# Performance work log

Measured on AMD Instinct MI355X. Metric: run time of the kernel, lower is better.

Reference implementation:

```python
import jax, jax.numpy as jnp
import numpy as np

NUM_EXPERTS = 8
K = 2
N_EMBD = 1024
HIDDEN = 4 * N_EMBD
BATCH = 2
SEQ = 1024
LB_SCALE = 0.01
NOISY_STD = 1.0
INIT_S = 0.02


def setup_inputs() -> dict:
    key = jax.random.key(0)
    ks = jax.random.split(key, 8)
    D, H, E = N_EMBD, HIDDEN, NUM_EXPERTS
    return {
        "x": jax.random.normal(ks[0], (BATCH, SEQ, D), jnp.float32),
        "noise": jax.random.normal(ks[1], (BATCH, SEQ, E), jnp.float32),  # torch.randn_like(logits)
        "gate_w": jax.random.normal(ks[2], (E, D), jnp.float32) * INIT_S,
        "noise_weight": jnp.zeros((E,), jnp.float32),  # initialized to zeros in the module
        "w1": jax.random.normal(ks[3], (E, H, D), jnp.float32) * INIT_S,
        "b1": jnp.zeros((E, H), jnp.float32),
        "w2": jax.random.normal(ks[4], (E, H, D), jnp.float32) * INIT_S,
        "b2": jnp.zeros((E, H), jnp.float32),
        "wp": jax.random.normal(ks[5], (E, D, H), jnp.float32) * INIT_S,
        "bp": jnp.zeros((E, D), jnp.float32),
    }


def reference(x, noise, gate_w, noise_weight, w1, b1, w2, b2, wp, bp):
    B, S, D = x.shape
    E = gate_w.shape[0]

    # ---- TopKGateParallel ----
    logits = jnp.einsum('bsd,ed->bse', x, gate_w)           # [B,S,E]
    gate_weights = jax.nn.softmax(logits, axis=-1)
    gw_mean = gate_weights.reshape(-1, E).mean(axis=0)       # [E]
    load_balance_loss = jnp.mean((gw_mean - 1.0 / E) ** 2) * LB_SCALE  # mse vs uniform

    logits_noisy = logits + (noise * NOISY_STD) * noise_weight
    top_v, top_i = jax.lax.top_k(logits_noisy, K)            # [B,S,K]
    # scatter top-k logits into a -inf sea, then softmax -> zeros at non-topk slots
    topk_mask = jnp.sum(jax.nn.one_hot(top_i, E, dtype=jnp.float32), axis=-2) > 0  # [B,S,E]
    sparse_logits = jnp.where(topk_mask, logits_noisy, -jnp.inf)
    top_k_gated_weights = jax.nn.softmax(sparse_logits, axis=-1)  # [B,S,E]

    # ---- expert compute + weighted combine (world_size=1: all experts local) ----
    x_flat = x.reshape(B * S, D)                              # [T,D]
    w_flat = top_k_gated_weights.reshape(B * S, E)            # [T,E]
    y = jnp.zeros_like(x_flat)
    for e in range(E):  # fixed small set of experts
        h = x_flat @ w1[e].T + b1[e]                          # [T,H]
        g = x_flat @ w2[e].T + b2[e]                          # [T,H]
        out_e = (h * jax.nn.silu(g)) @ wp[e].T + bp[e]        # [T,D]
        y = y + w_flat[:, e:e + 1] * out_e
    y = y.reshape(B, S, D)
    return y, load_balance_loss
```

## Files before the change

kernel.cpp:

```cpp
#include <hip/hip_runtime.h>

#define TOK 2048
#define DIM 1024
#define HID 4096
#define NE 8
#define KSPLIT 4
#define T2MAX 12

typedef unsigned short u16;
typedef __attribute__((ext_vector_type(8))) short s16x8;
typedef __attribute__((ext_vector_type(4))) short s16x4;
typedef __attribute__((ext_vector_type(4))) float f32x4;

__device__ __forceinline__ u16 f2b(float f) {
  unsigned u = __builtin_bit_cast(unsigned, f);
  unsigned r = (u + 0x7fffu + ((u >> 16) & 1u)) >> 16;
  return (u16)r;
}

__device__ __forceinline__ void gld_lds16(const void* g, void* l) {
  __builtin_amdgcn_global_load_lds((const __attribute__((address_space(1))) void*)g,
                                   (__attribute__((address_space(3))) void*)l, 16, 0, 0);
}

__global__ __launch_bounds__(256) void k_gate(const float* __restrict__ x,
    const float* __restrict__ noise, const float* __restrict__ gw,
    const float* __restrict__ nw,
    int* __restrict__ tok_e, float* __restrict__ tok_w,
    int* __restrict__ bhist, float* __restrict__ bgw, u16* __restrict__ x16) {
  const int wid = threadIdx.x >> 6, lane = threadIdx.x & 63;
  const int t = blockIdx.x * 4 + wid;
  const float* xr = x + (size_t)t * DIM + lane * 16;
  float acc[NE];
#pragma unroll
  for (int e = 0; e < NE; ++e) acc[e] = 0.f;
  u16 xb[16];
#pragma unroll
  for (int j = 0; j < 4; ++j) {
    float4 xv = *(const float4*)(xr + j * 4);
    xb[j * 4 + 0] = f2b(xv.x); xb[j * 4 + 1] = f2b(xv.y);
    xb[j * 4 + 2] = f2b(xv.z); xb[j * 4 + 3] = f2b(xv.w);
#pragma unroll
    for (int e = 0; e < NE; ++e) {
      float4 gv = *(const float4*)(gw + e * DIM + lane * 16 + j * 4);
      acc[e] += xv.x * gv.x + xv.y * gv.y + xv.z * gv.z + xv.w * gv.w;
    }
  }
  *(s16x8*)(x16 + (size_t)t * DIM + lane * 16) = *(const s16x8*)xb;
  *(s16x8*)(x16 + (size_t)t * DIM + lane * 16 + 8) = *(const s16x8*)(xb + 8);
#pragma unroll
  for (int e = 0; e < NE; ++e) {
#pragma unroll
    for (int off = 32; off >= 1; off >>= 1) acc[e] += __shfl_xor(acc[e], off);
  }
  float m = acc[0];
#pragma unroll
  for (int e = 1; e < NE; ++e) m = fmaxf(m, acc[e]);
  float p[NE]; float s = 0.f;
#pragma unroll
  for (int e = 0; e < NE; ++e) { p[e] = expf(acc[e] - m); s += p[e]; }
  float inv = 1.f / s;
  float v[NE];
#pragma unroll
  for (int e = 0; e < NE; ++e) v[e] = acc[e] + noise[t * NE + e] * nw[e];
  float v0 = -3.4e38f, v1 = -3.4e38f; int i0 = 0, i1 = 0;
#pragma unroll
  for (int e = 0; e < NE; ++e) {
    float ve = v[e];
    if (ve > v0) { v1 = v0; i1 = i0; v0 = ve; i0 = e; }
    else if (ve > v1) { v1 = ve; i1 = e; }
  }
  float e1 = expf(v1 - v0);
  float den = 1.f + e1;
  float w0 = 1.f / den, w1v = e1 / den;

  __shared__ float pl[4][NE];
  __shared__ int el[4][2];
  if (lane == 0) {
#pragma unroll
    for (int e = 0; e < NE; ++e) pl[wid][e] = p[e] * inv;
    el[wid][0] = i0; el[wid][1] = i1;
    tok_e[t * 2] = i0; tok_e[t * 2 + 1] = i1;
    tok_w[t * 2] = w0; tok_w[t * 2 + 1] = w1v;
  }
  __syncthreads();
  if (threadIdx.x < NE) {
    const int e = threadIdx.x;
    float ps = pl[0][e] + pl[1][e] + pl[2][e] + pl[3][e];
    int h = 0;
#pragma unroll
    for (int j = 0; j < 4; ++j) {
      h += (el[j][0] == e);
      h += (el[j][1] == e);
    }
    bgw[blockIdx.x * NE + e] = ps;
    bhist[blockIdx.x * NE + e] = h;
  }
}

__global__ __launch_bounds__(512) void k_scan(const int* __restrict__ bhist,
    const float* __restrict__ bgw, int* __restrict__ blk_off, int* __restrict__ prefix,
    int* __restrict__ counts, int* __restrict__ tile_tab, float* __restrict__ loss_out) {
  const int i = threadIdx.x, lane = i & 63, wv = i >> 6;
  __shared__ int wsum[8];
  __shared__ float wfs[8];
  __shared__ int etot[8];
  __shared__ float fsum[8];
  for (int e = 0; e < NE; ++e) {
    int v = bhist[i * NE + e];
    int sc = v;
#pragma unroll
    for (int off = 1; off < 64; off <<= 1) {
      int u = __shfl_up(sc, off);
      if (lane >= off) sc += u;
    }
    float f = bgw[i * NE + e];
#pragma unroll
    for (int off = 32; off >= 1; off >>= 1) f += __shfl_xor(f, off);
    if (lane == 63) wsum[wv] = sc;
    if (lane == 0) wfs[wv] = f;
    __syncthreads();
    int base = 0;
    for (int w2 = 0; w2 < wv; ++w2) base += wsum[w2];
    blk_off[i * NE + e] = base + sc - v;
    if (i == 0) {
      float tf = 0.f;
      for (int w2 = 0; w2 < 8; ++w2) tf += wfs[w2];
      fsum[e] = tf;
    }
    if (i == 511) etot[e] = base + sc;
    __syncthreads();
  }
  if (i == 0) {
    int sacc = 0;
    float l = 0.f;
    int tt = 0;
#pragma unroll
    for (int e = 0; e < NE; ++e) { prefix[e] = sacc; counts[e] = etot[e]; sacc += etot[e]; }
    for (int e = 0; e < NE; ++e) {
      const int nmt = (etot[e] + 511) >> 9;
      for (int m2 = 0; m2 < nmt; ++m2) tile_tab[tt++] = (e << 16) | m2;
    }
    for (; tt < T2MAX; ++tt) tile_tab[tt] = -1;
#pragma unroll
    for (int e = 0; e < NE; ++e) {
      float d = fsum[e] * (1.f / TOK) - 0.125f;
      l += d * d;
    }
    *loss_out = l * (0.01f / NE);
  }
}

__global__ __launch_bounds__(256) void k_build(const int* __restrict__ tok_e,
    const float* __restrict__ tok_w, const int* __restrict__ prefix,
    const int* __restrict__ blk_off, int* __restrict__ ent, float* __restrict__ entw,
    int* __restrict__ inv) {
  const int t = blockIdx.x * 256 + threadIdx.x;
  const int g = t >> 2;
  const int base = (t & 3) * 2;
  int ee[8];
#pragma unroll
  for (int j = 0; j < 8; ++j) ee[j] = tok_e[g * 8 + j];
#pragma unroll
  for (int s = 0; s < 2; ++s) {
    const int e = ee[base + s];
    int rank = 0;
#pragma unroll
    for (int j = 0; j < 8; ++j) rank += (j < base + s) && (ee[j] == e);
    const int idx = prefix[e] + blk_off[g * NE + e] + rank;
    ent[idx] = t * 2 + s;
    entw[idx] = tok_w[t * 2 + s];
    inv[t * 2 + s] = idx;
  }
}

__global__ __launch_bounds__(512) void k_gemm1f(const u16* __restrict__ x16,
    const float* __restrict__ w1, const float* __restrict__ w2,
    const float* __restrict__ b1, const float* __restrict__ b2,
    const int* __restrict__ ent, const int* __restrict__ counts,
    const int* __restrict__ prefix, const int* __restrict__ tile_tab,
    u16* __restrict__ act) {
  const int tt = tile_tab[blockIdx.y];
  if (tt < 0) return;
  const int e = tt >> 16, mt = tt & 0xffff, nt = blockIdx.x;
  const int cnt = counts[e];
  const int pfx = prefix[e];
  const int tid = threadIdx.x, w = tid >> 6, l = tid & 63;

  __shared__ u16 smem[2][20480];

  const int cA = (tid & 3) ^ ((tid >> 3) & 3);
  const u16* srcA[4]; int dstA[4];
#pragma unroll
  for (int q = 0; q < 4; ++q) {
    const int rr = q * 128 + (tid >> 2);
    int g = mt * 512 + rr; if (g >= cnt) g = cnt - 1;
    srcA[q] = x16 + (size_t)(ent[pfx + g] >> 1) * DIM + cA * 8;
    dstA[q] = q * 4096 + tid * 8;
  }
  const int rB = tid >> 3, cB = tid & 7;
  const float* pB1 = w1 + ((size_t)e * HID + nt * 64 + rB) * DIM + cB * 4;
  const float* pB2 = w2 + ((size_t)e * HID + nt * 64 + rB) * DIM + cB * 4;
  const int pos8 = cB ^ (((rB >> 1) & 3) << 1);
  const int wb1 = 16384 + rB * 32 + pos8 * 4;
  const int wb2 = 18432 + rB * 32 + pos8 * 4;

  const int xs = ((l >> 4) ^ ((l >> 1) & 3)) * 8;
  const int ra = (w * 64 + (l & 15)) * 32;
  const int rbb = (l & 15) * 32;

  f32x4 acc1[4][4], acc2[4][4];
#pragma unroll
  for (int m = 0; m < 4; ++m)
#pragma unroll
    for (int n = 0; n < 4; ++n) {
      acc1[m][n] = (f32x4){0.f, 0.f, 0.f, 0.f};
      acc2[m][n] = (f32x4){0.f, 0.f, 0.f, 0.f};
    }

  f32x4 a0_, a1_;
  f32x4 b0_, b1_;

  auto LOADB = [&](f32x4& r0_, f32x4& r1_, int kt) {
    r0_ = *(const f32x4*)(pB1 + kt * 32);
    r1_ = *(const f32x4*)(pB2 + kt * 32);
  };
  auto STAGEA = [&](int buf, int kt) {
#pragma unroll
    for (int q = 0; q < 4; ++q) gld_lds16(srcA[q] + kt * 32, &smem[buf][dstA[q]]);
  };
  auto WRITEB = [&](int buf, const f32x4& r0_, const f32x4& r1_) {
    u16 u[8];
    u[0] = f2b(r0_[0]); u[1] = f2b(r0_[1]); u[2] = f2b(r0_[2]); u[3] = f2b(r0_[3]);
    u[4] = f2b(r1_[0]); u[5] = f2b(r1_[1]); u[6] = f2b(r1_[2]); u[7] = f2b(r1_[3]);
    *(s16x4*)&smem[buf][wb1] = *(const s16x4*)u;
    *(s16x4*)&smem[buf][wb2] = *(const s16x4*)(u + 4);
  };
  auto MSTEP = [&](int buf) {
    const u16* S = &smem[buf][0];
    s16x8 af[4];
#pragma unroll
    for (int m = 0; m < 4; ++m) af[m] = *(const s16x8*)(S + ra + m * 512 + xs);
    __builtin_amdgcn_s_setprio(1);
#pragma unroll
    for (int n = 0; n < 4; ++n) {
      s16x8 bf1 = *(const s16x8*)(S + 16384 + n * 512 + rbb + xs);
      s16x8 bf2 = *(const s16x8*)(S + 18432 + n * 512 + rbb + xs);
#pragma unroll
      for (int m = 0; m < 4; ++m) {
        acc1[m][n] = __builtin_amdgcn_mfma_f32_16x16x32_bf16(af[m], bf1, acc1[m][n], 0, 0, 0);
        acc2[m][n] = __builtin_amdgcn_mfma_f32_16x16x32_bf16(af[m], bf2, acc2[m][n], 0, 0, 0);
      }
    }
    __builtin_amdgcn_s_setprio(0);
  };

  const int NT = DIM / 32;
  LOADB(a0_, a1_, 0);
  STAGEA(0, 0);
  LOADB(b0_, b1_, 1);
  asm volatile("s_waitcnt vmcnt(2)" ::: "memory");
  __builtin_amdgcn_sched_barrier(0);
  WRITEB(0, a0_, a1_);
  STAGEA(1, 1);
  asm volatile("s_waitcnt lgkmcnt(0)" ::: "memory");
  __builtin_amdgcn_sched_barrier(0);
  __builtin_amdgcn_s_barrier();

  for (int kt = 0; kt < NT; kt += 2) {
    if (kt + 2 < NT) LOADB(a0_, a1_, kt + 2);
    MSTEP(0);
    __builtin_amdgcn_s_barrier();
    if (kt + 2 < NT) asm volatile("s_waitcnt vmcnt(2)" ::: "memory");
    else             asm volatile("s_waitcnt vmcnt(0)" ::: "memory");
    __builtin_amdgcn_sched_barrier(0);
    WRITEB(1, b0_, b1_);
    if (kt + 2 < NT) STAGEA(0, kt + 2);
    asm volatile("s_waitcnt lgkmcnt(0)" ::: "memory");
    __builtin_amdgcn_sched_barrier(0);
    __builtin_amdgcn_s_barrier();
    if (kt + 3 < NT) LOADB(b0_, b1_, kt + 3);
    MSTEP(1);
    if (kt + 2 < NT) {
      __builtin_amdgcn_s_barrier();
      if (kt + 3 < NT) asm volatile("s_waitcnt vmcnt(2)" ::: "memory");
      else             asm volatile("s_waitcnt vmcnt(0)" ::: "memory");
      __builtin_amdgcn_sched_barrier(0);
      WRITEB(0, a0_, a1_);
      if (kt + 3 < NT) STAGEA(1, kt + 3);
      asm volatile("s_waitcnt lgkmcnt(0)" ::: "memory");
      __builtin_amdgcn_sched_barrier(0);
      __builtin_amdgcn_s_barrier();
    }
  }

#pragma unroll
  for (int n = 0; n < 4; ++n) {
    const int col = nt * 64 + n * 16 + (l & 15);
    const float bb1 = b1[(size_t)e * HID + col];
    const float bb2 = b2[(size_t)e * HID + col];
#pragma unroll
    for (int m = 0; m < 4; ++m) {
#pragma unroll
      for (int r = 0; r < 4; ++r) {
        const int row = mt * 512 + w * 64 + m * 16 + (l >> 4) * 4 + r;
        if (row < cnt) {
          float h = acc1[m][n][r] + bb1;
          float g = acc2[m][n][r] + bb2;
          float a = h * g / (1.f + expf(-g));
          act[(size_t)(pfx + row) * HID + col] = f2b(a);
        }
      }
    }
  }
}

__global__ __launch_bounds__(512) void k_gemm2f(const u16* __restrict__ act,
    const float* __restrict__ wp, const float* __restrict__ bp,
    const float* __restrict__ entw, const int* __restrict__ counts,
    const int* __restrict__ prefix, const int* __restrict__ tile_tab,
    float* __restrict__ yp) {
  const int tt = tile_tab[blockIdx.y];
  if (tt < 0) return;
  const int e = tt >> 16, mt = tt & 0xffff;
  const int sk = blockIdx.z, nt = blockIdx.x;
  const int cnt = counts[e];
  const int pfx = prefix[e];
  const int tid = threadIdx.x, w = tid >> 6, l = tid & 63;

  __shared__ u16 smem[2][20480];

  const int kbase = sk * (HID / KSPLIT);
  const int cA = (tid & 3) ^ ((tid >> 3) & 3);
  const u16* srcA[4]; int dstA[4];
#pragma unroll
  for (int q = 0; q < 4; ++q) {
    const int rr = q * 128 + (tid >> 2);
    int g = mt * 512 + rr; if (g >= cnt) g = cnt - 1;
    srcA[q] = act + (size_t)(pfx + g) * HID + kbase + cA * 8;
    dstA[q] = q * 4096 + tid * 8;
  }
  const int rB = tid >> 2;
  const float* pB = wp + ((size_t)e * DIM + nt * 128 + rB) * HID + kbase + (tid & 3) * 8;
  const int c0 = ((tid & 3) * 2) ^ (((rB >> 1) & 3) << 1);
  const int c1 = ((tid & 3) * 2 + 1) ^ (((rB >> 1) & 3) << 1);
  const int wbB = 16384 + rB * 32;

  const int xs = ((l >> 4) ^ ((l >> 1) & 3)) * 8;
  const int ra = (w * 64 + (l & 15)) * 32;
  const int rbb = (l & 15) * 32;

  f32x4 acc[4][8];
#pragma unroll
  for (int m = 0; m < 4; ++m)
#pragma unroll
    for (int n = 0; n < 8; ++n) acc[m][n] = (f32x4){0.f, 0.f, 0.f, 0.f};

  f32x4 a0_, a1_;
  f32x4 b0_, b1_;

  auto LOADB = [&](f32x4& r0_, f32x4& r1_, int kt) {
    r0_ = *(const f32x4*)(pB + kt * 32);
    r1_ = *(const f32x4*)(pB + kt * 32 + 4);
  };
  auto STAGEA = [&](int buf, int kt) {
#pragma unroll
    for (int q = 0; q < 4; ++q) gld_lds16(srcA[q] + kt * 32, &smem[buf][dstA[q]]);
  };
  auto WRITEB = [&](int buf, const f32x4& r0_, const f32x4& r1_) {
    u16 u[8];
    u[0] = f2b(r0_[0]); u[1] = f2b(r0_[1]); u[2] = f2b(r0_[2]); u[3] = f2b(r0_[3]);
    u[4] = f2b(r1_[0]); u[5] = f2b(r1_[1]); u[6] = f2b(r1_[2]); u[7] = f2b(r1_[3]);
    *(s16x4*)&smem[buf][wbB + c0 * 4] = *(const s16x4*)u;
    *(s16x4*)&smem[buf][wbB + c1 * 4] = *(const s16x4*)(u + 4);
  };
  auto MSTEP = [&](int buf) {
    const u16* S = &smem[buf][0];
    s16x8 af[4];
#pragma unroll
    for (int m = 0; m < 4; ++m) af[m] = *(const s16x8*)(S + ra + m * 512 + xs);
    __builtin_amdgcn_s_setprio(1);
#pragma unroll
    for (int n = 0; n < 8; ++n) {
      s16x8 bf = *(const s16x8*)(S + 16384 + n * 512 + rbb + xs);
#pragma unroll
      for (int m = 0; m < 4; ++m)
        acc[m][n] = __builtin_amdgcn_mfma_f32_16x16x32_bf16(af[m], bf, acc[m][n], 0, 0, 0);
    }
    __builtin_amdgcn_s_setprio(0);
  };

  const int NT = HID / KSPLIT / 32;
  LOADB(a0_, a1_, 0);
  STAGEA(0, 0);
  LOADB(b0_, b1_, 1);
  asm volatile("s_waitcnt vmcnt(2)" ::: "memory");
  __builtin_amdgcn_sched_barrier(0);
  WRITEB(0, a0_, a1_);
  STAGEA(1, 1);
  asm volatile("s_waitcnt lgkmcnt(0)" ::: "memory");
  __builtin_amdgcn_sched_barrier(0);
  __builtin_amdgcn_s_barrier();

  for (int kt = 0; kt < NT; kt += 2) {
    if (kt + 2 < NT) LOADB(a0_, a1_, kt + 2);
    MSTEP(0);
    __builtin_amdgcn_s_barrier();
    if (kt + 2 < NT) asm volatile("s_waitcnt vmcnt(2)" ::: "memory");
    else             asm volatile("s_waitcnt vmcnt(0)" ::: "memory");
    __builtin_amdgcn_sched_barrier(0);
    WRITEB(1, b0_, b1_);
    if (kt + 2 < NT) STAGEA(0, kt + 2);
    asm volatile("s_waitcnt lgkmcnt(0)" ::: "memory");
    __builtin_amdgcn_sched_barrier(0);
    __builtin_amdgcn_s_barrier();
    if (kt + 3 < NT) LOADB(b0_, b1_, kt + 3);
    MSTEP(1);
    if (kt + 2 < NT) {
      __builtin_amdgcn_s_barrier();
      if (kt + 3 < NT) asm volatile("s_waitcnt vmcnt(2)" ::: "memory");
      else             asm volatile("s_waitcnt vmcnt(0)" ::: "memory");
      __builtin_amdgcn_sched_barrier(0);
      WRITEB(0, a0_, a1_);
      if (kt + 3 < NT) STAGEA(1, kt + 3);
      asm volatile("s_waitcnt lgkmcnt(0)" ::: "memory");
      __builtin_amdgcn_sched_barrier(0);
      __builtin_amdgcn_s_barrier();
    }
  }

#pragma unroll
  for (int n = 0; n < 8; ++n) {
    const int col = nt * 128 + n * 16 + (l & 15);
    const float bpv = (sk == 0) ? bp[(size_t)e * DIM + col] : 0.f;
#pragma unroll
    for (int m = 0; m < 4; ++m) {
#pragma unroll
      for (int r = 0; r < 4; ++r) {
        const int row = mt * 512 + w * 64 + m * 16 + (l >> 4) * 4 + r;
        if (row < cnt) {
          const int idx = pfx + row;
          yp[((size_t)sk * (TOK * 2) + idx) * DIM + col] = entw[idx] * (acc[m][n][r] + bpv);
        }
      }
    }
  }
}

__global__ __launch_bounds__(256) void k_final(const float* __restrict__ yp,
    const int* __restrict__ inv, float* __restrict__ out) {
  const int t = blockIdx.x;
  const int d = threadIdx.x * 4;
  const int i0 = inv[t * 2], i1 = inv[t * 2 + 1];
  float4 s = {0.f, 0.f, 0.f, 0.f};
#pragma unroll
  for (int sk = 0; sk < KSPLIT; ++sk) {
    float4 a = *(const float4*)(yp + ((size_t)sk * (TOK * 2) + i0) * DIM + d);
    float4 b = *(const float4*)(yp + ((size_t)sk * (TOK * 2) + i1) * DIM + d);
    s.x += a.x + b.x; s.y += a.y + b.y; s.z += a.z + b.z; s.w += a.w + b.w;
  }
  *(float4*)(out + (size_t)t * DIM + d) = s;
}

extern "C" void kernel_launch(void* const* d_in, const int* in_sizes, int n_in,
                              void* d_out, int out_size, void* d_ws, size_t ws_size,
                              hipStream_t stream) {
  const float* x      = (const float*)d_in[0];
  const float* noise  = (const float*)d_in[1];
  const float* gate_w = (const float*)d_in[2];
  const float* nw     = (const float*)d_in[3];
  const float* w1     = (const float*)d_in[4];
  const float* b1     = (const float*)d_in[5];
  const float* w2     = (const float*)d_in[6];
  const float* b2     = (const float*)d_in[7];
  const float* wp     = (const float*)d_in[8];
  const float* bp     = (const float*)d_in[9];
  float* out = (float*)d_out;
  char* ws = (char*)d_ws;

  const size_t SZ_X16 = (size_t)TOK * DIM * 2;
  const size_t SZ_ACT = (size_t)TOK * 2 * HID * 2;
  const size_t SZ_YP  = (size_t)KSPLIT * TOK * 2 * DIM * 4;

  u16* x16  = (u16*)ws;
  u16* act  = (u16*)(ws + SZ_X16);
  float* yp = (float*)(ws + SZ_X16 + SZ_ACT);
  char* meta = ws + SZ_X16 + SZ_ACT + SZ_YP;
  int*   tok_e    = (int*)(meta);
  float* tok_w    = (float*)(meta + 16384);
  int*   ent      = (int*)(meta + 32768);
  float* entw     = (float*)(meta + 49152);
  int*   bhist    = (int*)(meta + 65536);
  float* bgw      = (float*)(meta + 81920);
  int*   blk_off  = (int*)(meta + 98304);
  int*   inv      = (int*)(meta + 114688);
  int*   counts   = (int*)(meta + 131072);
  int*   prefix   = (int*)(meta + 131072 + 64);
  int*   tile_tab = (int*)(meta + 131072 + 128);

  k_gate<<<TOK / 4, 256, 0, stream>>>(x, noise, gate_w, nw, tok_e, tok_w, bhist, bgw, x16);
  k_scan<<<1, 512, 0, stream>>>(bhist, bgw, blk_off, prefix, counts, tile_tab,
                                out + (size_t)TOK * DIM);
  k_build<<<TOK / 256, 256, 0, stream>>>(tok_e, tok_w, prefix, blk_off, ent, entw, inv);
  k_gemm1f<<<dim3(HID / 64, T2MAX), 512, 0, stream>>>(x16, w1, w2, b1, b2, ent,
                                                      counts, prefix, tile_tab, act);
  k_gemm2f<<<dim3(DIM / 128, T2MAX, KSPLIT), 512, 0, stream>>>(act, wp, bp, entw,
                                                               counts, prefix, tile_tab, yp);
  k_final<<<TOK, 256, 0, stream>>>(yp, inv, out);
}
```

Baseline: 322.3 us.

## Triple-buffer LDS in both expert GEMMs with one barrier per k-step

```diff
diff --git a/kernel.cpp b/kernel.cpp
--- a/kernel.cpp
+++ b/kernel.cpp
@@ -5,7 +5,7 @@
 #define HID 4096
 #define NE 8
 #define KSPLIT 4
-#define T2MAX 12
+#define T2MAX 16
 
 typedef unsigned short u16;
 typedef __attribute__((ext_vector_type(8))) short s16x8;
@@ -139,7 +139,7 @@
     for (int e = 0; e < NE; ++e) { prefix[e] = sacc; counts[e] = etot[e]; sacc += etot[e]; }
     for (int e = 0; e < NE; ++e) {
       const int nmt = (etot[e] + 511) >> 9;
-      for (int m2 = 0; m2 < nmt; ++m2) tile_tab[tt++] = (e << 16) | m2;
+      for (int m2 = 0; m2 < nmt && tt < T2MAX; ++m2) tile_tab[tt++] = (e << 16) | m2;
     }
     for (; tt < T2MAX; ++tt) tile_tab[tt] = -1;
 #pragma unroll
@@ -187,23 +187,21 @@
   const int pfx = prefix[e];
   const int tid = threadIdx.x, w = tid >> 6, l = tid & 63;
 
-  __shared__ u16 smem[2][20480];
+  __shared__ u16 smem[61440];
 
   const int cA = (tid & 3) ^ ((tid >> 3) & 3);
-  const u16* srcA[4]; int dstA[4];
+  const u16* srcA[4];
 #pragma unroll
   for (int q = 0; q < 4; ++q) {
     const int rr = q * 128 + (tid >> 2);
     int g = mt * 512 + rr; if (g >= cnt) g = cnt - 1;
     srcA[q] = x16 + (size_t)(ent[pfx + g] >> 1) * DIM + cA * 8;
-    dstA[q] = q * 4096 + tid * 8;
   }
   const int rB = tid >> 3, cB = tid & 7;
   const float* pB1 = w1 + ((size_t)e * HID + nt * 64 + rB) * DIM + cB * 4;
   const float* pB2 = w2 + ((size_t)e * HID + nt * 64 + rB) * DIM + cB * 4;
   const int pos8 = cB ^ (((rB >> 1) & 3) << 1);
-  const int wb1 = 16384 + rB * 32 + pos8 * 4;
-  const int wb2 = 18432 + rB * 32 + pos8 * 4;
+  const int wbOff = rB * 32 + pos8 * 4;
 
   const int xs = ((l >> 4) ^ ((l >> 1) & 3)) * 8;
   const int ra = (w * 64 + (l & 15)) * 32;
@@ -218,81 +216,78 @@
       acc2[m][n] = (f32x4){0.f, 0.f, 0.f, 0.f};
     }
 
-  f32x4 a0_, a1_;
-  f32x4 b0_, b1_;
-
-  auto LOADB = [&](f32x4& r0_, f32x4& r1_, int kt) {
-    r0_ = *(const f32x4*)(pB1 + kt * 32);
-    r1_ = *(const f32x4*)(pB2 + kt * 32);
-  };
-  auto STAGEA = [&](int buf, int kt) {
-#pragma unroll
-    for (int q = 0; q < 4; ++q) gld_lds16(srcA[q] + kt * 32, &smem[buf][dstA[q]]);
-  };
-  auto WRITEB = [&](int buf, const f32x4& r0_, const f32x4& r1_) {
-    u16 u[8];
-    u[0] = f2b(r0_[0]); u[1] = f2b(r0_[1]); u[2] = f2b(r0_[2]); u[3] = f2b(r0_[3]);
-    u[4] = f2b(r1_[0]); u[5] = f2b(r1_[1]); u[6] = f2b(r1_[2]); u[7] = f2b(r1_[3]);
-    *(s16x4*)&smem[buf][wb1] = *(const s16x4*)u;
-    *(s16x4*)&smem[buf][wb2] = *(const s16x4*)(u + 4);
-  };
-  auto MSTEP = [&](int buf) {
-    const u16* S = &smem[buf][0];
-    s16x8 af[4];
-#pragma unroll
-    for (int m = 0; m < 4; ++m) af[m] = *(const s16x8*)(S + ra + m * 512 + xs);
-    __builtin_amdgcn_s_setprio(1);
-#pragma unroll
-    for (int n = 0; n < 4; ++n) {
-      s16x8 bf1 = *(const s16x8*)(S + 16384 + n * 512 + rbb + xs);
-      s16x8 bf2 = *(const s16x8*)(S + 18432 + n * 512 + rbb + xs);
-#pragma unroll
-      for (int m = 0; m < 4; ++m) {
-        acc1[m][n] = __builtin_amdgcn_mfma_f32_16x16x32_bf16(af[m], bf1, acc1[m][n], 0, 0, 0);
-        acc2[m][n] = __builtin_amdgcn_mfma_f32_16x16x32_bf16(af[m], bf2, acc2[m][n], 0, 0, 0);
-      }
-    }
-    __builtin_amdgcn_s_setprio(0);
-  };
+  f32x4 rA0, rA1;
+  f32x4 rB0, rB1;
+
+#define LB1(R0, R1, KT) { R0 = *(const f32x4*)(pB1 + (KT) * 32); R1 = *(const f32x4*)(pB2 + (KT) * 32); }
+#define ST1(NXT, KT) { _Pragma("unroll") for (int q = 0; q < 4; ++q) \
+    gld_lds16(srcA[q] + (KT) * 32, &smem[(NXT) * 16384 + q * 4096 + tid * 8]); }
+#define WB1(WBUF, R0, R1) { u16 u_[8]; \
+    u_[0] = f2b(R0[0]); u_[1] = f2b(R0[1]); u_[2] = f2b(R0[2]); u_[3] = f2b(R0[3]); \
+    u_[4] = f2b(R1[0]); u_[5] = f2b(R1[1]); u_[6] = f2b(R1[2]); u_[7] = f2b(R1[3]); \
+    *(s16x4*)&smem[49152 + (WBUF) * 4096 + wbOff] = *(const s16x4*)u_; \
+    *(s16x4*)&smem[49152 + (WBUF) * 4096 + 2048 + wbOff] = *(const s16x4*)(u_ + 4); }
+#define MS1(CUR) { s16x8 af_[4]; \
+    _Pragma("unroll") for (int m = 0; m < 4; ++m) \
+      af_[m] = *(const s16x8*)&smem[(CUR) * 16384 + ra + m * 512 + xs]; \
+    __builtin_amdgcn_s_setprio(1); \
+    _Pragma("unroll") for (int n = 0; n < 4; ++n) { \
+      s16x8 bf1_ = *(const s16x8*)&smem[49152 + (CUR) * 4096 + n * 512 + rbb + xs]; \
+      s16x8 bf2_ = *(const s16x8*)&smem[49152 + (CUR) * 4096 + 2048 + n * 512 + rbb + xs]; \
+      _Pragma("unroll") for (int m = 0; m < 4; ++m) { \
+        acc1[m][n] = __builtin_amdgcn_mfma_f32_16x16x32_bf16(af_[m], bf1_, acc1[m][n], 0, 0, 0); \
+        acc2[m][n] = __builtin_amdgcn_mfma_f32_16x16x32_bf16(af_[m], bf2_, acc2[m][n], 0, 0, 0); \
+      } \
+    } \
+    __builtin_amdgcn_s_setprio(0); }
+#define STEP1(S_, CUR, WB, NXT, RL0, RL1, RW0, RW1) \
+    LB1(RL0, RL1, (S_) + 2); \
+    asm volatile("s_waitcnt vmcnt(6)" ::: "memory"); \
+    __builtin_amdgcn_sched_barrier(0); \
+    WB1(WB, RW0, RW1); \
+    ST1(NXT, (S_) + 2); \
+    MS1(CUR); \
+    asm volatile("s_waitcnt lgkmcnt(0)" ::: "memory"); \
+    asm volatile("s_waitcnt vmcnt(6)" ::: "memory"); \
+    __builtin_amdgcn_sched_barrier(0); \
+    __builtin_amdgcn_s_barrier();
 
   const int NT = DIM / 32;
-  LOADB(a0_, a1_, 0);
-  STAGEA(0, 0);
-  LOADB(b0_, b1_, 1);
-  asm volatile("s_waitcnt vmcnt(2)" ::: "memory");
-  __builtin_amdgcn_sched_barrier(0);
-  WRITEB(0, a0_, a1_);
-  STAGEA(1, 1);
+  LB1(rA0, rA1, 0);
+  ST1(0, 0);
+  LB1(rB0, rB1, 1);
+  ST1(1, 1);
+  asm volatile("s_waitcnt vmcnt(10)" ::: "memory");
+  __builtin_amdgcn_sched_barrier(0);
+  WB1(0, rA0, rA1);
+  asm volatile("s_waitcnt vmcnt(6)" ::: "memory");
   asm volatile("s_waitcnt lgkmcnt(0)" ::: "memory");
   __builtin_amdgcn_sched_barrier(0);
   __builtin_amdgcn_s_barrier();
 
-  for (int kt = 0; kt < NT; kt += 2) {
-    if (kt + 2 < NT) LOADB(a0_, a1_, kt + 2);
-    MSTEP(0);
-    __builtin_amdgcn_s_barrier();
-    if (kt + 2 < NT) asm volatile("s_waitcnt vmcnt(2)" ::: "memory");
-    else             asm volatile("s_waitcnt vmcnt(0)" ::: "memory");
-    __builtin_amdgcn_sched_barrier(0);
-    WRITEB(1, b0_, b1_);
-    if (kt + 2 < NT) STAGEA(0, kt + 2);
-    asm volatile("s_waitcnt lgkmcnt(0)" ::: "memory");
-    __builtin_amdgcn_sched_barrier(0);
-    __builtin_amdgcn_s_barrier();
-    if (kt + 3 < NT) LOADB(b0_, b1_, kt + 3);
-    MSTEP(1);
-    if (kt + 2 < NT) {
-      __builtin_amdgcn_s_barrier();
-      if (kt + 3 < NT) asm volatile("s_waitcnt vmcnt(2)" ::: "memory");
-      else             asm volatile("s_waitcnt vmcnt(0)" ::: "memory");
-      __builtin_amdgcn_sched_barrier(0);
-      WRITEB(0, a0_, a1_);
-      if (kt + 3 < NT) STAGEA(1, kt + 3);
-      asm volatile("s_waitcnt lgkmcnt(0)" ::: "memory");
-      __builtin_amdgcn_sched_barrier(0);
-      __builtin_amdgcn_s_barrier();
-    }
-  }
+  for (int kt = 0; kt < NT - 2; kt += 6) {
+    STEP1(kt + 0, 0, 1, 2, rA0, rA1, rB0, rB1);
+    STEP1(kt + 1, 1, 2, 0, rB0, rB1, rA0, rA1);
+    STEP1(kt + 2, 2, 0, 1, rA0, rA1, rB0, rB1);
+    STEP1(kt + 3, 0, 1, 2, rB0, rB1, rA0, rA1);
+    STEP1(kt + 4, 1, 2, 0, rA0, rA1, rB0, rB1);
+    STEP1(kt + 5, 2, 0, 1, rB0, rB1, rA0, rA1);
+  }
+  asm volatile("s_waitcnt vmcnt(4)" ::: "memory");
+  __builtin_amdgcn_sched_barrier(0);
+  WB1(1, rB0, rB1);
+  MS1(0);
+  asm volatile("s_waitcnt lgkmcnt(0)" ::: "memory");
+  asm volatile("s_waitcnt vmcnt(0)" ::: "memory");
+  __builtin_amdgcn_sched_barrier(0);
+  __builtin_amdgcn_s_barrier();
+  MS1(1);
+
+#undef LB1
+#undef ST1
+#undef WB1
+#undef MS1
+#undef STEP1
 
 #pragma unroll
   for (int n = 0; n < 4; ++n) {
@@ -328,23 +323,22 @@
   const int pfx = prefix[e];
   const int tid = threadIdx.x, w = tid >> 6, l = tid & 63;
 
-  __shared__ u16 smem[2][20480];
+  __shared__ u16 smem[61440];
 
   const int kbase = sk * (HID / KSPLIT);
   const int cA = (tid & 3) ^ ((tid >> 3) & 3);
-  const u16* srcA[4]; int dstA[4];
+  const u16* srcA[4];
 #pragma unroll
   for (int q = 0; q < 4; ++q) {
     const int rr = q * 128 + (tid >> 2);
     int g = mt * 512 + rr; if (g >= cnt) g = cnt - 1;
     srcA[q] = act + (size_t)(pfx + g) * HID + kbase + cA * 8;
-    dstA[q] = q * 4096 + tid * 8;
   }
   const int rB = tid >> 2;
   const float* pB = wp + ((size_t)e * DIM + nt * 128 + rB) * HID + kbase + (tid & 3) * 8;
   const int c0 = ((tid & 3) * 2) ^ (((rB >> 1) & 3) << 1);
   const int c1 = ((tid & 3) * 2 + 1) ^ (((rB >> 1) & 3) << 1);
-  const int wbB = 16384 + rB * 32;
+  const int wbOff = rB * 32;
 
   const int xs = ((l >> 4) ^ ((l >> 1) & 3)) * 8;
   const int ra = (w * 64 + (l & 15)) * 32;
@@ -356,78 +350,75 @@
 #pragma unroll
     for (int n = 0; n < 8; ++n) acc[m][n] = (f32x4){0.f, 0.f, 0.f, 0.f};
 
-  f32x4 a0_, a1_;
-  f32x4 b0_, b1_;
-
-  auto LOADB = [&](f32x4& r0_, f32x4& r1_, int kt) {
-    r0_ = *(const f32x4*)(pB + kt * 32);
-    r1_ = *(const f32x4*)(pB + kt * 32 + 4);
-  };
-  auto STAGEA = [&](int buf, int kt) {
-#pragma unroll
-    for (int q = 0; q < 4; ++q) gld_lds16(srcA[q] + kt * 32, &smem[buf][dstA[q]]);
-  };
-  auto WRITEB = [&](int buf, const f32x4& r0_, const f32x4& r1_) {
-    u16 u[8];
-    u[0] = f2b(r0_[0]); u[1] = f2b(r0_[1]); u[2] = f2b(r0_[2]); u[3] = f2b(r0_[3]);
-    u[4] = f2b(r1_[0]); u[5] = f2b(r1_[1]); u[6] = f2b(r1_[2]); u[7] = f2b(r1_[3]);
-    *(s16x4*)&smem[buf][wbB + c0 * 4] = *(const s16x4*)u;
-    *(s16x4*)&smem[buf][wbB + c1 * 4] = *(const s16x4*)(u + 4);
-  };
-  auto MSTEP = [&](int buf) {
-    const u16* S = &smem[buf][0];
-    s16x8 af[4];
-#pragma unroll
-    for (int m = 0; m < 4; ++m) af[m] = *(const s16x8*)(S + ra + m * 512 + xs);
-    __builtin_amdgcn_s_setprio(1);
-#pragma unroll
-    for (int n = 0; n < 8; ++n) {
-      s16x8 bf = *(const s16x8*)(S + 16384 + n * 512 + rbb + xs);
-#pragma unroll
-      for (int m = 0; m < 4; ++m)
-        acc[m][n] = __builtin_amdgcn_mfma_f32_16x16x32_bf16(af[m], bf, acc[m][n], 0, 0, 0);
-    }
-    __builtin_amdgcn_s_setprio(0);
-  };
+  f32x4 rA0, rA1;
+  f32x4 rB0, rB1;
+
+#define LB2(R0, R1, KT) { R0 = *(const f32x4*)(pB + (KT) * 32); R1 = *(const f32x4*)(pB + (KT) * 32 + 4); }
+#define ST2(NXT, KT) { _Pragma("unroll") for (int q = 0; q < 4; ++q) \
+    gld_lds16(srcA[q] + (KT) * 32, &smem[(NXT) * 16384 + q * 4096 + tid * 8]); }
+#define WB2(WBUF, R0, R1) { u16 u_[8]; \
+    u_[0] = f2b(R0[0]); u_[1] = f2b(R0[1]); u_[2] = f2b(R0[2]); u_[3] = f2b(R0[3]); \
+    u_[4] = f2b(R1[0]); u_[5] = f2b(R1[1]); u_[6] = f2b(R1[2]); u_[7] = f2b(R1[3]); \
+    *(s16x4*)&smem[49152 + (WBUF) * 4096 + wbOff + c0 * 4] = *(const s16x4*)u_; \
+    *(s16x4*)&smem[49152 + (WBUF) * 4096 + wbOff + c1 * 4] = *(const s16x4*)(u_ + 4); }
+#define MS2(CUR) { s16x8 af_[4]; \
+    _Pragma("unroll") for (int m = 0; m < 4; ++m) \
+      af_[m] = *(const s16x8*)&smem[(CUR) * 16384 + ra + m * 512 + xs]; \
+    __builtin_amdgcn_s_setprio(1); \
+    _Pragma("unroll") for (int n = 0; n < 8; ++n) { \
+      s16x8 bf_ = *(const s16x8*)&smem[49152 + (CUR) * 4096 + n * 512 + rbb + xs]; \
+      _Pragma("unroll") for (int m = 0; m < 4; ++m) \
+        acc[m][n] = __builtin_amdgcn_mfma_f32_16x16x32_bf16(af_[m], bf_, acc[m][n], 0, 0, 0); \
+    } \
+    __builtin_amdgcn_s_setprio(0); }
+#define STEP2(S_, CUR, WB, NXT, RL0, RL1, RW0, RW1) \
+    LB2(RL0, RL1, (S_) + 2); \
+    asm volatile("s_waitcnt vmcnt(6)" ::: "memory"); \
+    __builtin_amdgcn_sched_barrier(0); \
+    WB2(WB, RW0, RW1); \
+    ST2(NXT, (S_) + 2); \
+    MS2(CUR); \
+    asm volatile("s_waitcnt lgkmcnt(0)" ::: "memory"); \
+    asm volatile("s_waitcnt vmcnt(6)" ::: "memory"); \
+    __builtin_amdgcn_sched_barrier(0); \
+    __builtin_amdgcn_s_barrier();
 
   const int NT = HID / KSPLIT / 32;
-  LOADB(a0_, a1_, 0);
-  STAGEA(0, 0);
-  LOADB(b0_, b1_, 1);
-  asm volatile("s_waitcnt vmcnt(2)" ::: "memory");
-  __builtin_amdgcn_sched_barrier(0);
-  WRITEB(0, a0_, a1_);
-  STAGEA(1, 1);
+  LB2(rA0, rA1, 0);
+  ST2(0, 0);
+  LB2(rB0, rB1, 1);
+  ST2(1, 1);
+  asm volatile("s_waitcnt vmcnt(10)" ::: "memory");
+  __builtin_amdgcn_sched_barrier(0);
+  WB2(0, rA0, rA1);
+  asm volatile("s_waitcnt vmcnt(6)" ::: "memory");
   asm volatile("s_waitcnt lgkmcnt(0)" ::: "memory");
   __builtin_amdgcn_sched_barrier(0);
   __builtin_amdgcn_s_barrier();
 
-  for (int kt = 0; kt < NT; kt += 2) {
-    if (kt + 2 < NT) LOADB(a0_, a1_, kt + 2);
-    MSTEP(0);
-    __builtin_amdgcn_s_barrier();
-    if (kt + 2 < NT) asm volatile("s_waitcnt vmcnt(2)" ::: "memory");
-    else             asm volatile("s_waitcnt vmcnt(0)" ::: "memory");
-    __builtin_amdgcn_sched_barrier(0);
-    WRITEB(1, b0_, b1_);
-    if (kt + 2 < NT) STAGEA(0, kt + 2);
-    asm volatile("s_waitcnt lgkmcnt(0)" ::: "memory");
-    __builtin_amdgcn_sched_barrier(0);
-    __builtin_amdgcn_s_barrier();
-    if (kt + 3 < NT) LOADB(b0_, b1_, kt + 3);
-    MSTEP(1);
-    if (kt + 2 < NT) {
-      __builtin_amdgcn_s_barrier();
-      if (kt + 3 < NT) asm volatile("s_waitcnt vmcnt(2)" ::: "memory");
-      else             asm volatile("s_waitcnt vmcnt(0)" ::: "memory");
-      __builtin_amdgcn_sched_barrier(0);
-      WRITEB(0, a0_, a1_);
-      if (kt + 3 < NT) STAGEA(1, kt + 3);
-      asm volatile("s_waitcnt lgkmcnt(0)" ::: "memory");
-      __builtin_amdgcn_sched_barrier(0);
-      __builtin_amdgcn_s_barrier();
-    }
-  }
+  for (int kt = 0; kt < NT - 2; kt += 6) {
+    STEP2(kt + 0, 0, 1, 2, rA0, rA1, rB0, rB1);
+    STEP2(kt + 1, 1, 2, 0, rB0, rB1, rA0, rA1);
+    STEP2(kt + 2, 2, 0, 1, rA0, rA1, rB0, rB1);
+    STEP2(kt + 3, 0, 1, 2, rB0, rB1, rA0, rA1);
+    STEP2(kt + 4, 1, 2, 0, rA0, rA1, rB0, rB1);
+    STEP2(kt + 5, 2, 0, 1, rB0, rB1, rA0, rA1);
+  }
+  asm volatile("s_waitcnt vmcnt(4)" ::: "memory");
+  __builtin_amdgcn_sched_barrier(0);
+  WB2(1, rB0, rB1);
+  MS2(0);
+  asm volatile("s_waitcnt lgkmcnt(0)" ::: "memory");
+  asm volatile("s_waitcnt vmcnt(0)" ::: "memory");
+  __builtin_amdgcn_sched_barrier(0);
+  __builtin_amdgcn_s_barrier();
+  MS2(1);
+
+#undef LB2
+#undef ST2
+#undef WB2
+#undef MS2
+#undef STEP2
 
 #pragma unroll
   for (int n = 0; n < 8; ++n) {
```

Result: slower. 350.2 us (+8.7%).
